# Performance work log

Measured on AMD Instinct MI355X. Metric: run time of the kernel, lower is better.

## Reference

```python
import jax, jax.numpy as jnp
import numpy as np

N_NODES = 50000
N_EDGES = 1600000
SLOPE = 0.01  # torch leaky_relu default negative_slope


def _lrelu(x):
    return jnp.where(x >= 0, x, SLOPE * x)


def _graph_conv(x, edge_index, w_rel, b_rel, w_root):
    # PyG GraphConv (aggr='add'): out_i = W_rel @ sum_{j->i} x_j + b_rel + W_root @ x_i
    src, dst = edge_index[0], edge_index[1]
    agg = jax.ops.segment_sum(x[src], dst, num_segments=x.shape[0])  # [N, F_in]
    return agg @ w_rel.T + b_rel + x @ w_root.T


def setup_inputs() -> dict:
    key = jax.random.key(0)
    ks = jax.random.split(key, 12)

    def glorot(k, shape):
        fan_in = shape[-1]
        return jax.random.normal(k, shape, dtype=jnp.float32) / np.sqrt(fan_in)

    x = jax.random.normal(ks[0], (N_NODES, 2048), dtype=jnp.float32)
    edge_index = jax.random.randint(ks[1], (2, N_EDGES), 0, N_NODES, dtype=jnp.int64)

    return {
        "x": x,
        "edge_index": edge_index,
        "lin1_w": glorot(ks[2], (128, 2048)),
        "lin1_b": jnp.zeros((128,), jnp.float32),
        "conv1_w_rel": glorot(ks[3], (64, 128)),
        "conv1_b_rel": jnp.zeros((64,), jnp.float32),
        "conv1_w_root": glorot(ks[4], (64, 128)),
        "conv4_w_rel": glorot(ks[5], (32, 64)),
        "conv4_b_rel": jnp.zeros((32,), jnp.float32),
        "conv4_w_root": glorot(ks[6], (32, 64)),
        "pos_w": glorot(ks[7], (3, 32)),
        "pos_b": jnp.zeros((3,), jnp.float32),
    }


def reference(x, edge_index, lin1_w, lin1_b, conv1_w_rel, conv1_b_rel,
              conv1_w_root, conv4_w_rel, conv4_b_rel, conv4_w_root,
              pos_w, pos_b):
    # dropout layers are identity at inference
    h = _lrelu(x @ lin1_w.T + lin1_b)                                  # [N, 128]
    h = _lrelu(_graph_conv(h, edge_index, conv1_w_rel, conv1_b_rel, conv1_w_root))  # [N, 64]
    h = _lrelu(_graph_conv(h, edge_index, conv4_w_rel, conv4_b_rel, conv4_w_root))  # [N, 32]
    position = h @ pos_w.T + pos_b                                     # [N, 3]
    return position
```

## Files before the change

kernel.cpp:

```cpp
#include <hip/hip_runtime.h>

#define N_NODES 50000
#define N_EDGES 1600000

typedef __attribute__((ext_vector_type(4))) float f32x4;
typedef __attribute__((ext_vector_type(8))) short bf16x8;
typedef unsigned short u16;

#define ABYTES 8192

__device__ __forceinline__ float lrelu(float x) { return x >= 0.f ? x : 0.01f * x; }

__device__ __forceinline__ u16 f2bf(float f) {
    union { float f; unsigned u; } v; v.f = f;
    unsigned u = v.u;
    u += 0x7fffu + ((u >> 16) & 1u);
    return (u16)(u >> 16);
}

__device__ __forceinline__ float bf2f(u16 v) {
    union { unsigned u; float f; } x; x.u = ((unsigned)v) << 16; return x.f;
}

__device__ __forceinline__ bf16x8 cvt8(float4 a, float4 b) {
    bf16x8 r;
    r[0] = (short)f2bf(a.x); r[1] = (short)f2bf(a.y);
    r[2] = (short)f2bf(a.z); r[3] = (short)f2bf(a.w);
    r[4] = (short)f2bf(b.x); r[5] = (short)f2bf(b.y);
    r[6] = (short)f2bf(b.z); r[7] = (short)f2bf(b.w);
    return r;
}

__launch_bounds__(256)
__global__ void k_prep(const float* __restrict__ W1,
                       const float* __restrict__ W2a, const float* __restrict__ W2b,
                       const float* __restrict__ W3a, const float* __restrict__ W3b,
                       u16* __restrict__ wf1, u16* __restrict__ wf2, u16* __restrict__ wf3,
                       int* __restrict__ deg)
{
    const int b = blockIdx.x;
    if (b < 1024) {
        int i = b * 256 + threadIdx.x;
        int e = i & 7, lane = (i >> 3) & 63, nf = (i >> 9) & 7, ks = i >> 12;
        int n = nf * 16 + (lane & 15);
        int k = ks * 32 + 8 * (lane >> 4) + e;
        wf1[i] = f2bf(W1[(size_t)n * 2048 + k]);
    } else if (b < 1088) {
        int i = (b - 1024) * 256 + threadIdx.x;
        int e = i & 7, lane = (i >> 3) & 63, nf = (i >> 9) & 7, ks = i >> 12;
        int n = nf * 16 + (lane & 15);
        int k = ks * 32 + 8 * (lane >> 4) + e;
        float v = (n < 64) ? W2a[(size_t)n * 128 + k] : W2b[(size_t)(n - 64) * 128 + k];
        wf2[i] = f2bf(v);
    } else if (b < 1104) {
        int i = (b - 1088) * 256 + threadIdx.x;
        int e = i & 7, lane = (i >> 3) & 63, nf = (i >> 9) & 3, ks = i >> 11;
        int n = nf * 16 + (lane & 15);
        int k = ks * 32 + 8 * (lane >> 4) + e;
        float v = (n < 32) ? W3a[(size_t)n * 64 + k] : W3b[(size_t)(n - 32) * 64 + k];
        wf3[i] = f2bf(v);
    } else {
        int i = (b - 1104) * 256 + threadIdx.x;
        if (i < N_NODES) deg[i] = 0;
    }
}

__launch_bounds__(256)
__global__ void k_hist(const int* __restrict__ ei, int* __restrict__ deg)
{
    const int stride = gridDim.x * 256;
    for (int e = blockIdx.x * 256 + threadIdx.x; e < N_EDGES; e += stride)
        atomicAdd(deg + ei[N_EDGES + e], 1);
}

__device__ __forceinline__ void compute_step(const char* slot, int lane, int wave,
                                             f32x4 acc[2][4])
{
    const int lrow = lane & 15;
    const int k16 = lane >> 4;
    const int rs = wave >> 1;
    const int ch = wave & 1;

    bf16x8 af[2];
#pragma unroll
    for (int st = 0; st < 2; st++) {
        const int row = rs * 32 + st * 16 + lrow;
        af[st] = *(const bf16x8*)(slot + row * 64 + ((k16 ^ (row & 3)) << 4));
    }
    bf16x8 bf[4];
#pragma unroll
    for (int j = 0; j < 4; j++)
        bf[j] = *(const bf16x8*)(slot + ABYTES + (ch * 4 + j) * 1024 + lane * 16);

#pragma unroll
    for (int st = 0; st < 2; st++)
#pragma unroll
        for (int j = 0; j < 4; j++)
            acc[st][j] = __builtin_amdgcn_mfma_f32_16x16x32_bf16(af[st], bf[j], acc[st][j], 0, 0, 0);
}

__launch_bounds__(512, 4)
__global__ void k_linf(const float* __restrict__ X, const u16* __restrict__ Wf1,
                       const u16* __restrict__ Wf2,
                       const float* __restrict__ Bv, const float* __restrict__ brel,
                       u16* __restrict__ t1, float* __restrict__ acc1)
{
    __shared__ __align__(16) char lds[2][16384];

    const int t = threadIdx.x, wave = t >> 6, lane = t & 63;
    const int lrow = lane & 15, lgrp = lane >> 4;
    const int m0 = blockIdx.x * 128;

    const int arow_l = t >> 2, kq = t & 3;
    int grow = m0 + arow_l; if (grow >= N_NODES) grow = N_NODES - 1;
    const float4* ap = (const float4*)(X + (size_t)grow * 2048);
    const bf16x8* bp = (const bf16x8*)Wf1;
    const int awr = arow_l * 64 + ((kq ^ (arow_l & 3)) << 4);
    const int bwr = ABYTES + t * 16;

    f32x4 acc[2][4];
#pragma unroll
    for (int st = 0; st < 2; st++)
#pragma unroll
        for (int j = 0; j < 4; j++) acc[st][j] = (f32x4)0.f;

    float4 cA0 = ap[kq * 2], cA1 = ap[kq * 2 + 1];
    bf16x8 cB = bp[t];
    float4 nA0 = ap[8 + kq * 2], nA1 = ap[8 + kq * 2 + 1];
    bf16x8 nB = bp[512 + t];
    *(bf16x8*)(lds[0] + awr) = cvt8(cA0, cA1);
    *(bf16x8*)(lds[0] + bwr) = cB;
    asm volatile("s_waitcnt lgkmcnt(0)" ::: "memory");
    __builtin_amdgcn_s_barrier();
    __builtin_amdgcn_sched_barrier(0);

#pragma unroll 2
    for (int s = 0; s < 62; s++) {
        float4 fA0 = ap[(s + 2) * 8 + kq * 2], fA1 = ap[(s + 2) * 8 + kq * 2 + 1];
        bf16x8 fB = bp[(s + 2) * 512 + t];

        compute_step(lds[s & 1], lane, wave, acc);
        __builtin_amdgcn_s_barrier();
        __builtin_amdgcn_sched_barrier(0);

        char* wslot = lds[(s + 1) & 1];
        *(bf16x8*)(wslot + awr) = cvt8(nA0, nA1);
        *(bf16x8*)(wslot + bwr) = nB;
        asm volatile("s_waitcnt lgkmcnt(0)" ::: "memory");
        __builtin_amdgcn_s_barrier();
        __builtin_amdgcn_sched_barrier(0);

        nA0 = fA0; nA1 = fA1; nB = fB;
    }
    compute_step(lds[0], lane, wave, acc);
    __builtin_amdgcn_s_barrier();
    __builtin_amdgcn_sched_barrier(0);
    *(bf16x8*)(lds[1] + awr) = cvt8(nA0, nA1);
    *(bf16x8*)(lds[1] + bwr) = nB;
    asm volatile("s_waitcnt lgkmcnt(0)" ::: "memory");
    __builtin_amdgcn_s_barrier();
    __builtin_amdgcn_sched_barrier(0);
    compute_step(lds[1], lane, wave, acc);
    __builtin_amdgcn_s_barrier();
    __builtin_amdgcn_sched_barrier(0);

    u16* hl = (u16*)&lds[0][0];
    {
        const int rs = wave >> 1, ch = wave & 1;
#pragma unroll
        for (int st = 0; st < 2; st++) {
#pragma unroll
            for (int j = 0; j < 4; j++) {
                const int col = ch * 64 + j * 16 + lrow;
                const float bias = Bv[col];
#pragma unroll
                for (int r = 0; r < 4; r++) {
                    const int row = rs * 32 + st * 16 + lgrp * 4 + r;
                    hl[row * 128 + (((col >> 3) ^ (row & 7)) << 3) + (col & 7)] =
                        f2bf(lrelu(acc[st][j][r] + bias));
                }
            }
        }
    }
    asm volatile("s_waitcnt lgkmcnt(0)" ::: "memory");
    __builtin_amdgcn_s_barrier();
    __builtin_amdgcn_sched_barrier(0);

    bf16x8 af2[4];
    {
        const int row = wave * 16 + lrow;
#pragma unroll
        for (int ks = 0; ks < 4; ks++) {
            const int chunk = ((ks << 2) + lgrp) ^ (row & 7);
            af2[ks] = *(const bf16x8*)(hl + row * 128 + (chunk << 3));
        }
    }
    f32x4 dacc[8];
#pragma unroll
    for (int i = 0; i < 8; i++) dacc[i] = (f32x4)0.f;
    const u16* bp2 = Wf2 + lane * 8;
#pragma unroll
    for (int ks = 0; ks < 4; ks++) {
#pragma unroll
        for (int nf = 0; nf < 8; nf++) {
            bf16x8 bf = *(const bf16x8*)(bp2 + ks * 4096 + nf * 512);
            dacc[nf] = __builtin_amdgcn_mfma_f32_16x16x32_bf16(af2[ks], bf, dacc[nf], 0, 0, 0);
        }
    }

    const int rbase = m0 + wave * 16 + lgrp * 4;
#pragma unroll
    for (int nf = 0; nf < 8; nf++) {
        const int col = nf * 16 + lrow;
#pragma unroll
        for (int r = 0; r < 4; r++) {
            const int row = rbase + r;
            if (row < N_NODES) {
                if (col < 64) t1[(size_t)row * 64 + col] = f2bf(dacc[nf][r]);
                else          acc1[(size_t)row * 64 + (col - 64)] = dacc[nf][r] + brel[col - 64];
            }
        }
    }
}

__launch_bounds__(256, 2)
__global__ void k_dualf2(const float* __restrict__ A, const u16* __restrict__ Wf,
                         const float* __restrict__ brel,
                         u16* __restrict__ t2, float* __restrict__ acc2)
{
    const int t = threadIdx.x, wave = t >> 6, lane = t & 63;
    const int lrow = lane & 15, lgrp = lane >> 4;
    const int arow = blockIdx.x * 64 + wave * 16 + lrow;
    const float* ap = A + (size_t)(arow < N_NODES ? arow : 0) * 64 + 8 * lgrp;
    const u16* bp = Wf + lane * 8;

    float4 a00 = *(const float4*)(ap + 0);
    float4 a01 = *(const float4*)(ap + 4);
    float4 a10 = *(const float4*)(ap + 32);
    float4 a11 = *(const float4*)(ap + 36);

    f32x4 acc[4];
#pragma unroll
    for (int i = 0; i < 4; i++) acc[i] = (f32x4)0.f;

    a00.x = lrelu(a00.x); a00.y = lrelu(a00.y); a00.z = lrelu(a00.z); a00.w = lrelu(a00.w);
    a01.x = lrelu(a01.x); a01.y = lrelu(a01.y); a01.z = lrelu(a01.z); a01.w = lrelu(a01.w);
    bf16x8 af0 = cvt8(a00, a01);
    a10.x = lrelu(a10.x); a10.y = lrelu(a10.y); a10.z = lrelu(a10.z); a10.w = lrelu(a10.w);
    a11.x = lrelu(a11.x); a11.y = lrelu(a11.y); a11.z = lrelu(a11.z); a11.w = lrelu(a11.w);
    bf16x8 af1 = cvt8(a10, a11);

#pragma unroll
    for (int nf = 0; nf < 4; nf++) {
        bf16x8 b0 = *(const bf16x8*)(bp + nf * 512);
        bf16x8 b1 = *(const bf16x8*)(bp + 2048 + nf * 512);
        acc[nf] = __builtin_amdgcn_mfma_f32_16x16x32_bf16(af0, b0, acc[nf], 0, 0, 0);
        acc[nf] = __builtin_amdgcn_mfma_f32_16x16x32_bf16(af1, b1, acc[nf], 0, 0, 0);
    }

    const int rbase = blockIdx.x * 64 + wave * 16 + lgrp * 4;
#pragma unroll
    for (int nf = 0; nf < 4; nf++) {
        const int col = nf * 16 + lrow;
#pragma unroll
        for (int r = 0; r < 4; r++) {
            const int row = rbase + r;
            if (row < N_NODES) {
                if (col < 32) t2[(size_t)row * 32 + col] = f2bf(acc[nf][r]);
                else          acc2[(size_t)row * 32 + (col - 32)] = acc[nf][r] + brel[col - 32];
            }
        }
    }
}

__launch_bounds__(256)
__global__ void k_scan1(const int* __restrict__ deg, int* __restrict__ tmp,
                        int* __restrict__ bsum)
{
    __shared__ int sm[256];
    const int tid = threadIdx.x;
    const int i = blockIdx.x * 256 + tid;
    int d = (i < N_NODES) ? deg[i] : 0;
    sm[tid] = d;
    __syncthreads();
#pragma unroll
    for (int off = 1; off < 256; off <<= 1) {
        int v = (tid >= off) ? sm[tid - off] : 0;
        __syncthreads();
        sm[tid] += v;
        __syncthreads();
    }
    if (i < N_NODES) tmp[i] = sm[tid];
    if (tid == 255) bsum[blockIdx.x] = sm[255];
}

__launch_bounds__(256)
__global__ void k_scan2p(const int* __restrict__ bsum, int* __restrict__ boff, int nb)
{
    __shared__ int sm[256];
    const int tid = threadIdx.x;
    int v = (tid < nb) ? bsum[tid] : 0;
    sm[tid] = v;
    __syncthreads();
#pragma unroll
    for (int off = 1; off < 256; off <<= 1) {
        int u = (tid >= off) ? sm[tid - off] : 0;
        __syncthreads();
        sm[tid] += u;
        __syncthreads();
    }
    if (tid < nb) boff[tid] = sm[tid] - v;
}

__launch_bounds__(256)
__global__ void k_scan3(const int* __restrict__ tmp, const int* __restrict__ boff,
                        const int* __restrict__ deg, int* __restrict__ ro,
                        int* __restrict__ cur)
{
    const int i = blockIdx.x * 256 + threadIdx.x;
    if (i < N_NODES) {
        int incl = tmp[i] + boff[i >> 8];
        ro[i + 1] = incl;
        cur[i] = incl - deg[i];
    }
    if (i == 0) ro[0] = 0;
}

__launch_bounds__(256)
__global__ void k_fill(const int* __restrict__ ei, int* __restrict__ cur,
                       int* __restrict__ csr)
{
    const int stride = gridDim.x * 256;
    for (int e = blockIdx.x * 256 + threadIdx.x; e < N_EDGES; e += stride) {
        const int dst = ei[N_EDGES + e];
        const int p = atomicAdd(cur + dst, 1);
        csr[p] = ei[e];
    }
}

__launch_bounds__(256)
__global__ void k_gather64(const int* __restrict__ ro, const int* __restrict__ csr,
                           const u16* __restrict__ t, float* __restrict__ acc)
{
    const int wid = (blockIdx.x << 2) | (threadIdx.x >> 6);
    if (wid >= N_NODES) return;
    const int lane = threadIdx.x & 63;
    const int s = ro[wid], e = ro[wid + 1];
    float a = acc[(size_t)wid * 64 + lane];
    int i = s;
    for (; i + 8 <= e; i += 8) {
        int s0 = csr[i], s1 = csr[i + 1], s2 = csr[i + 2], s3 = csr[i + 3];
        int s4 = csr[i + 4], s5 = csr[i + 5], s6 = csr[i + 6], s7 = csr[i + 7];
        u16 v0 = t[(size_t)s0 * 64 + lane], v1 = t[(size_t)s1 * 64 + lane];
        u16 v2 = t[(size_t)s2 * 64 + lane], v3 = t[(size_t)s3 * 64 + lane];
        u16 v4 = t[(size_t)s4 * 64 + lane], v5 = t[(size_t)s5 * 64 + lane];
        u16 v6 = t[(size_t)s6 * 64 + lane], v7 = t[(size_t)s7 * 64 + lane];
        a += bf2f(v0); a += bf2f(v1); a += bf2f(v2); a += bf2f(v3);
        a += bf2f(v4); a += bf2f(v5); a += bf2f(v6); a += bf2f(v7);
    }
    for (; i < e; ++i) a += bf2f(t[(size_t)csr[i] * 64 + lane]);
    acc[(size_t)wid * 64 + lane] = a;
}

__launch_bounds__(256)
__global__ void k_gpos(const int* __restrict__ ro, const int* __restrict__ csr,
                       const u16* __restrict__ t, const float* __restrict__ acc2,
                       const float* __restrict__ PW, const float* __restrict__ PB,
                       float* __restrict__ out)
{
    const int wid = (blockIdx.x << 2) | (threadIdx.x >> 6);
    if (wid >= N_NODES) return;
    const int lane = threadIdx.x & 63;
    const int half = lane >> 5, f = lane & 31;
    const int s = ro[wid], e = ro[wid + 1];
    float a = 0.f;
    int i = s;
    for (; i + 8 <= e; i += 8) {
        int s0 = csr[i + half], s1 = csr[i + 2 + half];
        int s2 = csr[i + 4 + half], s3 = csr[i + 6 + half];
        u16 v0 = t[(size_t)s0 * 32 + f], v1 = t[(size_t)s1 * 32 + f];
        u16 v2 = t[(size_t)s2 * 32 + f], v3 = t[(size_t)s3 * 32 + f];
        a += bf2f(v0); a += bf2f(v1); a += bf2f(v2); a += bf2f(v3);
    }
    for (; i < e; i += 2) {
        int idx = i + half;
        if (idx < e) a += bf2f(t[(size_t)csr[idx] * 32 + f]);
    }
    a += __shfl_xor(a, 32, 64);

    float v = lrelu(acc2[(size_t)wid * 32 + f] + a);
    float p0 = v * PW[f], p1 = v * PW[32 + f], p2 = v * PW[64 + f];
#pragma unroll
    for (int off = 16; off >= 1; off >>= 1) {
        p0 += __shfl_xor(p0, off, 64);
        p1 += __shfl_xor(p1, off, 64);
        p2 += __shfl_xor(p2, off, 64);
    }
    if (lane == 0) {
        out[(size_t)wid * 3 + 0] = p0 + PB[0];
        out[(size_t)wid * 3 + 1] = p1 + PB[1];
        out[(size_t)wid * 3 + 2] = p2 + PB[2];
    }
}

extern "C" void kernel_launch(void* const* d_in, const int* in_sizes, int n_in,
                              void* d_out, int out_size, void* d_ws, size_t ws_size,
                              hipStream_t stream)
{
    const float* x        = (const float*)d_in[0];
    const int*   ei       = (const int*)d_in[1];
    const float* lin1_w   = (const float*)d_in[2];
    const float* lin1_b   = (const float*)d_in[3];
    const float* c1_wrel  = (const float*)d_in[4];
    const float* c1_brel  = (const float*)d_in[5];
    const float* c1_wroot = (const float*)d_in[6];
    const float* c4_wrel  = (const float*)d_in[7];
    const float* c4_brel  = (const float*)d_in[8];
    const float* c4_wroot = (const float*)d_in[9];
    const float* pos_w    = (const float*)d_in[10];
    const float* pos_b    = (const float*)d_in[11];
    float* out = (float*)d_out;

    char* base = (char*)d_ws;
    u16*   t1b  = (u16*)base;
    float* acc1 = (float*)(base + 6400000);
    u16*   t2b  = (u16*)(base + 19200000);
    float* acc2 = (float*)(base + 22400000);
    u16*   wf1  = (u16*)(base + 28800000);
    u16*   wf2  = wf1 + 262144;
    u16*   wf3  = wf2 + 16384;
    int*   ibase = (int*)(wf3 + 4096);
    const int NPAD = ((N_NODES + 255) / 256) * 256;
    int* deg  = ibase;
    int* tmp  = deg  + NPAD;
    int* ro   = tmp  + NPAD;
    int* cur  = ro   + NPAD;
    int* bsum = cur  + NPAD;
    int* boff = bsum + 256;
    int* csr  = boff + 256;
    const int NB = (N_NODES + 255) / 256;

    hipLaunchKernelGGL(k_prep, dim3(1104 + NB), dim3(256), 0, stream,
                       lin1_w, c1_wrel, c1_wroot, c4_wrel, c4_wroot,
                       wf1, wf2, wf3, deg);
    hipLaunchKernelGGL(k_hist, dim3(1024), dim3(256), 0, stream, ei, deg);
    hipLaunchKernelGGL(k_scan1, dim3(NB), dim3(256), 0, stream, deg, tmp, bsum);
    hipLaunchKernelGGL(k_scan2p, dim3(1), dim3(256), 0, stream, bsum, boff, NB);
    hipLaunchKernelGGL(k_scan3, dim3(NB), dim3(256), 0, stream, tmp, boff, deg, ro, cur);
    hipLaunchKernelGGL(k_fill, dim3(1024), dim3(256), 0, stream, ei, cur, csr);

    hipLaunchKernelGGL(k_linf, dim3((N_NODES + 127) / 128), dim3(512), 0, stream,
                       x, wf1, wf2, lin1_b, c1_brel, t1b, acc1);
    hipLaunchKernelGGL(k_gather64, dim3((N_NODES + 3) / 4), dim3(256), 0, stream,
                       ro, csr, t1b, acc1);
    hipLaunchKernelGGL(k_dualf2, dim3((N_NODES + 63) / 64), dim3(256), 0, stream,
                       acc1, wf3, c4_brel, t2b, acc2);
    hipLaunchKernelGGL(k_gpos, dim3((N_NODES + 3) / 4), dim3(256), 0, stream,
                       ro, csr, t2b, acc2, pos_w, pos_b, out);
}
```

Before: 397.9 us.

## Triple-buffer LDS in lin1 GEMM with one barrier per step and 64-row tiles

After: 423.2 us. 6.4% more time.

```diff
diff --git a/kernel.cpp b/kernel.cpp
--- a/kernel.cpp
+++ b/kernel.cpp
@@ -7,7 +7,7 @@
 typedef __attribute__((ext_vector_type(8))) short bf16x8;
 typedef unsigned short u16;
 
-#define ABYTES 8192
+#define SLOT_BYTES 12288
 
 __device__ __forceinline__ float lrelu(float x) { return x >= 0.f ? x : 0.01f * x; }
 
@@ -85,12 +85,12 @@
 #pragma unroll
     for (int st = 0; st < 2; st++) {
         const int row = rs * 32 + st * 16 + lrow;
-        af[st] = *(const bf16x8*)(slot + row * 64 + ((k16 ^ (row & 3)) << 4));
+        af[st] = *(const bf16x8*)(slot + row * 64 + ((k16 ^ ((row >> 1) & 3)) << 4));
     }
     bf16x8 bf[4];
 #pragma unroll
     for (int j = 0; j < 4; j++)
-        bf[j] = *(const bf16x8*)(slot + ABYTES + (ch * 4 + j) * 1024 + lane * 16);
+        bf[j] = *(const bf16x8*)(slot + 4096 + (ch * 4 + j) * 1024 + lane * 16);
 
 #pragma unroll
     for (int st = 0; st < 2; st++)
@@ -99,24 +99,24 @@
             acc[st][j] = __builtin_amdgcn_mfma_f32_16x16x32_bf16(af[st], bf[j], acc[st][j], 0, 0, 0);
 }
 
-__launch_bounds__(512, 4)
+__launch_bounds__(256, 4)
 __global__ void k_linf(const float* __restrict__ X, const u16* __restrict__ Wf1,
                        const u16* __restrict__ Wf2,
                        const float* __restrict__ Bv, const float* __restrict__ brel,
                        u16* __restrict__ t1, float* __restrict__ acc1)
 {
-    __shared__ __align__(16) char lds[2][16384];
+    __shared__ __align__(16) char lds[3][SLOT_BYTES];
 
     const int t = threadIdx.x, wave = t >> 6, lane = t & 63;
     const int lrow = lane & 15, lgrp = lane >> 4;
-    const int m0 = blockIdx.x * 128;
+    const int m0 = blockIdx.x * 64;
 
     const int arow_l = t >> 2, kq = t & 3;
     int grow = m0 + arow_l; if (grow >= N_NODES) grow = N_NODES - 1;
     const float4* ap = (const float4*)(X + (size_t)grow * 2048);
     const bf16x8* bp = (const bf16x8*)Wf1;
-    const int awr = arow_l * 64 + ((kq ^ (arow_l & 3)) << 4);
-    const int bwr = ABYTES + t * 16;
+    const int awr = arow_l * 64 + ((kq ^ ((arow_l >> 1) & 3)) << 4);
+    const int bwr = 4096 + t * 32;
 
     f32x4 acc[2][4];
 #pragma unroll
@@ -124,43 +124,48 @@
 #pragma unroll
         for (int j = 0; j < 4; j++) acc[st][j] = (f32x4)0.f;
 
-    float4 cA0 = ap[kq * 2], cA1 = ap[kq * 2 + 1];
-    bf16x8 cB = bp[t];
-    float4 nA0 = ap[8 + kq * 2], nA1 = ap[8 + kq * 2 + 1];
-    bf16x8 nB = bp[512 + t];
-    *(bf16x8*)(lds[0] + awr) = cvt8(cA0, cA1);
-    *(bf16x8*)(lds[0] + bwr) = cB;
+    float4 wA0, wA1; bf16x8 wB0, wB1;
+    float4 iA0, iA1; bf16x8 iB0, iB1;
+    {
+        float4 a00 = ap[0 * 8 + kq * 2], a01 = ap[0 * 8 + kq * 2 + 1];
+        bf16x8 b00 = bp[0 * 512 + t * 2], b01 = bp[0 * 512 + t * 2 + 1];
+        float4 a10 = ap[1 * 8 + kq * 2], a11 = ap[1 * 8 + kq * 2 + 1];
+        bf16x8 b10 = bp[1 * 512 + t * 2], b11 = bp[1 * 512 + t * 2 + 1];
+        wA0 = ap[2 * 8 + kq * 2]; wA1 = ap[2 * 8 + kq * 2 + 1];
+        wB0 = bp[2 * 512 + t * 2]; wB1 = bp[2 * 512 + t * 2 + 1];
+        *(bf16x8*)(lds[0] + awr) = cvt8(a00, a01);
+        *(bf16x8*)(lds[0] + bwr) = b00;
+        *(bf16x8*)(lds[0] + bwr + 16) = b01;
+        *(bf16x8*)(lds[1] + awr) = cvt8(a10, a11);
+        *(bf16x8*)(lds[1] + bwr) = b10;
+        *(bf16x8*)(lds[1] + bwr + 16) = b11;
+    }
     asm volatile("s_waitcnt lgkmcnt(0)" ::: "memory");
     __builtin_amdgcn_s_barrier();
     __builtin_amdgcn_sched_barrier(0);
 
-#pragma unroll 2
-    for (int s = 0; s < 62; s++) {
-        float4 fA0 = ap[(s + 2) * 8 + kq * 2], fA1 = ap[(s + 2) * 8 + kq * 2 + 1];
-        bf16x8 fB = bp[(s + 2) * 512 + t];
-
-        compute_step(lds[s & 1], lane, wave, acc);
-        __builtin_amdgcn_s_barrier();
-        __builtin_amdgcn_sched_barrier(0);
-
-        char* wslot = lds[(s + 1) & 1];
-        *(bf16x8*)(wslot + awr) = cvt8(nA0, nA1);
-        *(bf16x8*)(wslot + bwr) = nB;
+#pragma unroll 3
+    for (int s = 0; s < 63; s++) {
+        if (s < 61) {
+            iA0 = ap[(s + 3) * 8 + kq * 2];
+            iA1 = ap[(s + 3) * 8 + kq * 2 + 1];
+            iB0 = bp[(s + 3) * 512 + t * 2];
+            iB1 = bp[(s + 3) * 512 + t * 2 + 1];
+        }
+        compute_step(lds[s % 3], lane, wave, acc);
+        if (s < 62) {
+            char* ws = lds[(s + 2) % 3];
+            *(bf16x8*)(ws + awr) = cvt8(wA0, wA1);
+            *(bf16x8*)(ws + bwr) = wB0;
+            *(bf16x8*)(ws + bwr + 16) = wB1;
+        }
         asm volatile("s_waitcnt lgkmcnt(0)" ::: "memory");
         __builtin_amdgcn_s_barrier();
         __builtin_amdgcn_sched_barrier(0);
-
-        nA0 = fA0; nA1 = fA1; nB = fB;
+        wA0 = iA0; wA1 = iA1; wB0 = iB0; wB1 = iB1;
     }
     compute_step(lds[0], lane, wave, acc);
-    __builtin_amdgcn_s_barrier();
-    __builtin_amdgcn_sched_barrier(0);
-    *(bf16x8*)(lds[1] + awr) = cvt8(nA0, nA1);
-    *(bf16x8*)(lds[1] + bwr) = nB;
     asm volatile("s_waitcnt lgkmcnt(0)" ::: "memory");
-    __builtin_amdgcn_s_barrier();
-    __builtin_amdgcn_sched_barrier(0);
-    compute_step(lds[1], lane, wave, acc);
     __builtin_amdgcn_s_barrier();
     __builtin_amdgcn_sched_barrier(0);
 
@@ -449,7 +454,7 @@
     hipLaunchKernelGGL(k_scan3, dim3(NB), dim3(256), 0, stream, tmp, boff, deg, ro, cur);
     hipLaunchKernelGGL(k_fill, dim3(1024), dim3(256), 0, stream, ei, cur, csr);
 
-    hipLaunchKernelGGL(k_linf, dim3((N_NODES + 127) / 128), dim3(512), 0, stream,
+    hipLaunchKernelGGL(k_linf, dim3((N_NODES + 63) / 64), dim3(256), 0, stream,
                        x, wf1, wf2, lin1_b, c1_brel, t1b, acc1);
     hipLaunchKernelGGL(k_gather64, dim3((N_NODES + 3) / 4), dim3(256), 0, stream,
                        ro, csr, t1b, acc1);
```
